# Performance work log

Measured on AMD Instinct MI355X. Metric: run time of the kernel, lower is better.

The kernel has to match this reference:

```python
import jax, jax.numpy as jnp
import numpy as np

# Model dims (from MambaLayer: Mamba2(d_model=256, d_state=128, d_conv=4, expand=2, headdim=64))
D_MODEL = 256
D_INNER = 512
D_STATE = 128
NHEADS = 8
HEADDIM = 64
D_CONV = 4
CONV_DIM = D_INNER + 2 * D_STATE          # 768
D_IN_PROJ = 2 * D_INNER + 2 * D_STATE + NHEADS  # 1288
ATT_HEADS = 8
MLP_HID = 4 * D_MODEL
NUM_CLASSES = 2


def _mamba2(x, in_proj_w, conv_w, conv_b, dt_bias, A_log, D_param, norm_w, out_proj_w):
    """Mamba2 forward (SSD selective scan), ngroups=1, no in_proj/out_proj bias."""
    b, L, _ = x.shape
    zxbcdt = x @ in_proj_w.T                                   # (b,L,1288)
    z = zxbcdt[..., :D_INNER]                                   # gate
    xBC = zxbcdt[..., D_INNER:D_INNER + CONV_DIM]
    dt = jax.nn.softplus(zxbcdt[..., -NHEADS:] + dt_bias)       # (b,L,h)
    # depthwise causal conv1d (kernel 4) + SiLU
    xpad = jnp.pad(xBC, ((0, 0), (D_CONV - 1, 0), (0, 0)))
    xBC = sum(conv_w[:, k] * xpad[:, k:k + L, :] for k in range(D_CONV)) + conv_b
    xBC = jax.nn.silu(xBC)
    xs = xBC[..., :D_INNER].reshape(b, L, NHEADS, HEADDIM)      # (b,L,h,p)
    Bm = xBC[..., D_INNER:D_INNER + D_STATE]                    # (b,L,n)
    Cm = xBC[..., D_INNER + D_STATE:]                           # (b,L,n)
    dA = jnp.exp(dt * (-jnp.exp(A_log)))                        # (b,L,h)

    def step(h_prev, inp):
        dA_t, dt_t, B_t, C_t, x_t = inp                         # (b,h),(b,h),(b,n),(b,n),(b,h,p)
        h = h_prev * dA_t[..., None, None] + (dt_t[..., None] * x_t)[..., None] * B_t[:, None, None, :]
        return h, jnp.einsum('bhpn,bn->bhp', h, C_t)

    tfirst = lambda a: jnp.moveaxis(a, 1, 0)
    h0 = jnp.zeros((b, NHEADS, HEADDIM, D_STATE), x.dtype)
    _, ys = jax.lax.scan(step, h0, (tfirst(dA), tfirst(dt), tfirst(Bm), tfirst(Cm), tfirst(xs)))
    y = jnp.moveaxis(ys, 0, 1) + D_param[None, None, :, None] * xs
    # gated RMSNorm then out projection
    y = y.reshape(b, L, D_INNER) * jax.nn.silu(z)
    y = y * jax.lax.rsqrt(jnp.mean(y * y, -1, keepdims=True) + 1e-5) * norm_w
    return y @ out_proj_w.T


def _cross_attn(x, ctx, wq, wk, wv, wo, wo_b, w1, b1, ln_w, ln_b, w2, b2):
    """CrossModalAttention.forward: attn -> out_proj -> Mlp (no residual, per source)."""
    b, t, c = x.shape
    hd = c // ATT_HEADS
    heads = lambda a: a.reshape(b, -1, ATT_HEADS, hd).transpose(0, 2, 1, 3)
    q, k, v = heads(x @ wq.T), heads(ctx @ wk.T), heads(ctx @ wv.T)
    att = jax.nn.softmax(jnp.einsum('bhxd,bhyd->bhxy', q, k) * (hd ** -0.5), axis=-1)
    o = jnp.einsum('bhxy,bhyd->bhxd', att, v).transpose(0, 2, 1, 3).reshape(b, t, c)
    o = o @ wo.T + wo_b
    h = jax.nn.gelu(o @ w1.T + b1, approximate=False)
    mu = jnp.mean(h, -1, keepdims=True)
    var = jnp.mean((h - mu) ** 2, -1, keepdims=True)
    h = (h - mu) * jax.lax.rsqrt(var + 1e-5) * ln_w + ln_b
    return h @ w2.T + b2


def setup_inputs() -> dict:
    key = jax.random.key(0)
    ks = iter(jax.random.split(key, 32))
    f32 = jnp.float32
    w = lambda *s: jax.random.normal(next(ks), s, f32) * 0.02
    return {
        'x': jax.random.normal(next(ks), (2, 2048, D_MODEL), f32),
        'context': jax.random.normal(next(ks), (2, 2048, D_MODEL), f32),
        'in_proj_w': w(D_IN_PROJ, D_MODEL),
        'conv_w': w(CONV_DIM, D_CONV),
        'conv_b': jnp.zeros((CONV_DIM,), f32),
        'dt_bias': jax.random.normal(next(ks), (NHEADS,), f32) * 0.5,
        'A_log': jnp.log(jnp.linspace(1.0, 16.0, NHEADS).astype(f32)),
        'D_param': jnp.ones((NHEADS,), f32),
        'norm_w': jnp.ones((D_INNER,), f32),
        'out_proj_w': w(D_MODEL, D_INNER),
        'wq': w(D_MODEL, D_MODEL),
        'wk': w(D_MODEL, D_MODEL),
        'wv': w(D_MODEL, D_MODEL),
        'wo': w(D_MODEL, D_MODEL),
        'wo_b': jnp.zeros((D_MODEL,), f32),
        'w1': w(MLP_HID, D_MODEL),
        'b1': jnp.zeros((MLP_HID,), f32),
        'ln_w': jnp.ones((MLP_HID,), f32),
        'ln_b': jnp.zeros((MLP_HID,), f32),
        'w2': w(D_MODEL, MLP_HID),
        'b2': jnp.zeros((D_MODEL,), f32),
        'head_w': w(NUM_CLASSES, D_MODEL),
        'head_b': jnp.zeros((NUM_CLASSES,), f32),
    }


def reference(x, context, in_proj_w, conv_w, conv_b, dt_bias, A_log, D_param, norm_w, out_proj_w,
              wq, wk, wv, wo, wo_b, w1, b1, ln_w, ln_b, w2, b2, head_w, head_b):
    h = x + _mamba2(x, in_proj_w, conv_w, conv_b, dt_bias, A_log, D_param, norm_w, out_proj_w)
    h = _cross_attn(h, context, wq, wk, wv, wo, wo_b, w1, b1, ln_w, ln_b, w2, b2)
    # ClsHead: mean-pool over tokens, linear to classes
    return jnp.mean(h, axis=1) @ head_w.T + head_b
```

## Files before the change

kernel.cpp:

```cpp
#include <hip/hip_runtime.h>
#include <hip/hip_bf16.h>
#include <math.h>

#define DEVFN __device__ __forceinline__

constexpr int BATCH = 2;
constexpr int SEQ   = 2048;
constexpr int DM    = 256;
constexpr int DI    = 512;
constexpr int DSTATE= 128;
constexpr int NH    = 8;
constexpr int HD    = 64;
constexpr int CDIM  = 768;
constexpr int DPROJ = 1288;
constexpr int MTOK  = BATCH*SEQ;
constexpr int HID   = 1024;
constexpr int CHUNK = 32;
constexpr int NCHUNK= SEQ/CHUNK;
constexpr int NSPLIT= 4;
constexpr int KVLEN = SEQ/NSPLIT;

typedef __bf16 bf16x8 __attribute__((ext_vector_type(8)));
typedef __bf16 bf16x4 __attribute__((ext_vector_type(4)));
typedef __bf16 bf16x2 __attribute__((ext_vector_type(2)));
typedef float  f32x4  __attribute__((ext_vector_type(4)));

DEVFN float gelu_exact(float x){ return 0.5f*x*(1.f+erff(x*0.70710678118654752f)); }
DEVFN float silu_f(float x){ return x/(1.f+expf(-x)); }

DEVFN bf16x8 pack8(float4 a, float4 b){
  bf16x8 r;
  r[0]=(__bf16)a.x; r[1]=(__bf16)a.y; r[2]=(__bf16)a.z; r[3]=(__bf16)a.w;
  r[4]=(__bf16)b.x; r[5]=(__bf16)b.y; r[6]=(__bf16)b.z; r[7]=(__bf16)b.w;
  return r;
}
DEVFN f32x4 mfma16(bf16x8 a, bf16x8 b, f32x4 c){
  return __builtin_amdgcn_mfma_f32_16x16x32_bf16(a, b, c, 0, 0, 0);
}

template<int ACT, bool HASBIAS, bool AF32>
__global__ __launch_bounds__(256)
void gemm128(const void* __restrict__ Av, const float* __restrict__ W,
             const float* __restrict__ bias, __bf16* __restrict__ C,
             int M, int N, int K)
{
  __shared__ __bf16 As[128][40];
  __shared__ __bf16 Ws[128][40];
  const int tid = threadIdx.x;
  const int bm = blockIdx.x * 128, bn = blockIdx.y * 128;
  const int wv = tid >> 6, lane = tid & 63;
  const int quad = lane >> 4, mr = lane & 15;
  const int wm = (wv >> 1) * 64, wn = (wv & 1) * 64;
  const int srow = tid >> 2;
  const int skc  = (tid & 3) * 8;

  const float*  af0 = (const float*)Av + (size_t)(bm + srow)*K + skc;
  const float*  af1 = (const float*)Av + (size_t)(bm + srow + 64)*K + skc;
  const __bf16* ab0 = (const __bf16*)Av + (size_t)(bm + srow)*K + skc;
  const __bf16* ab1 = (const __bf16*)Av + (size_t)(bm + srow + 64)*K + skc;
  const bool wok0 = (bn + srow) < N;
  const bool wok1 = (bn + srow + 64) < N;
  const float* wp0 = W + (size_t)(bn + srow)*K + skc;
  const float* wp1 = W + (size_t)(bn + srow + 64)*K + skc;

  bf16x8 A0, A1;
  if (AF32){
    A0 = pack8(*(const float4*)af0, *(const float4*)(af0+4));
    A1 = pack8(*(const float4*)af1, *(const float4*)(af1+4));
  } else {
    A0 = *(const bf16x8*)ab0;
    A1 = *(const bf16x8*)ab1;
  }
  float4 z4 = make_float4(0,0,0,0);
  float4 W00 = wok0 ? *(const float4*)wp0     : z4;
  float4 W01 = wok0 ? *(const float4*)(wp0+4) : z4;
  float4 W10 = wok1 ? *(const float4*)wp1     : z4;
  float4 W11 = wok1 ? *(const float4*)(wp1+4) : z4;

  f32x4 acc[4][4];
  #pragma unroll
  for (int i=0;i<4;i++)
    #pragma unroll
    for (int j=0;j<4;j++) acc[i][j] = f32x4{0.f,0.f,0.f,0.f};

  for (int k0 = 0; k0 < K; k0 += 32) {
    __syncthreads();
    *(bf16x8*)&As[srow   ][skc] = A0;
    *(bf16x8*)&As[srow+64][skc] = A1;
    *(bf16x8*)&Ws[srow   ][skc] = pack8(W00, W01);
    *(bf16x8*)&Ws[srow+64][skc] = pack8(W10, W11);
    __syncthreads();
    if (k0 + 32 < K){
      int kn = k0 + 32;
      if (AF32){
        A0 = pack8(*(const float4*)(af0+kn), *(const float4*)(af0+kn+4));
        A1 = pack8(*(const float4*)(af1+kn), *(const float4*)(af1+kn+4));
      } else {
        A0 = *(const bf16x8*)(ab0+kn);
        A1 = *(const bf16x8*)(ab1+kn);
      }
      W00 = wok0 ? *(const float4*)(wp0+kn)   : z4;
      W01 = wok0 ? *(const float4*)(wp0+kn+4) : z4;
      W10 = wok1 ? *(const float4*)(wp1+kn)   : z4;
      W11 = wok1 ? *(const float4*)(wp1+kn+4) : z4;
    }
    bf16x8 afr[4], bfr[4];
    #pragma unroll
    for (int i=0;i<4;i++) afr[i] = *(const bf16x8*)&As[wm + i*16 + mr][quad*8];
    #pragma unroll
    for (int j=0;j<4;j++) bfr[j] = *(const bf16x8*)&Ws[wn + j*16 + mr][quad*8];
    #pragma unroll
    for (int i=0;i<4;i++)
      #pragma unroll
      for (int j=0;j<4;j++)
        acc[i][j] = mfma16(afr[i], bfr[j], acc[i][j]);
  }

  #pragma unroll
  for (int j=0;j<4;j++){
    int col = bn + wn + j*16 + mr;
    if (col >= N) continue;
    float bb = HASBIAS ? bias[col] : 0.f;
    #pragma unroll
    for (int i=0;i<4;i++){
      #pragma unroll
      for (int reg=0; reg<4; reg++){
        int row = bm + wm + i*16 + quad*4 + reg;
        float vv = acc[i][j][reg] + bb;
        if (ACT == 1) vv = gelu_exact(vv);
        C[(size_t)row*N + col] = (__bf16)vv;
      }
    }
  }
}

__global__ __launch_bounds__(256)
void gemm_outproj(const __bf16* __restrict__ A, const float* __restrict__ W,
                  const float* __restrict__ residf, __bf16* __restrict__ Cb,
                  int M, int N, int K)
{
  __shared__ __bf16 As[64][40];
  __shared__ __bf16 Ws[64][40];
  const int tid = threadIdx.x;
  const int bm = blockIdx.x*64, bn = blockIdx.y*64;
  const int w = tid >> 6, lane = tid & 63;
  const int quad = lane >> 4, mr = lane & 15;
  const int wm = (w >> 1) * 32, wn = (w & 1) * 32;
  const int srow = tid >> 2, skc = (tid & 3) * 8;

  const __bf16* ap = A + (size_t)(bm + srow)*K + skc;
  const float*  wp = W + (size_t)(bn + srow)*K + skc;
  bf16x8 a0 = *(const bf16x8*)ap;
  float4 w0 = *(const float4*)wp, w1 = *(const float4*)(wp+4);

  f32x4 acc[2][2];
  #pragma unroll
  for (int i=0;i<2;i++)
    #pragma unroll
    for (int j=0;j<2;j++) acc[i][j] = f32x4{0.f,0.f,0.f,0.f};

  for (int k0 = 0; k0 < K; k0 += 32){
    __syncthreads();
    *(bf16x8*)&As[srow][skc] = a0;
    *(bf16x8*)&Ws[srow][skc] = pack8(w0, w1);
    __syncthreads();
    if (k0 + 32 < K){
      a0 = *(const bf16x8*)(ap+k0+32);
      w0 = *(const float4*)(wp+k0+32); w1 = *(const float4*)(wp+k0+36);
    }
    bf16x8 af[2], bfr[2];
    af[0]  = *(const bf16x8*)&As[wm      + mr][quad*8];
    af[1]  = *(const bf16x8*)&As[wm + 16 + mr][quad*8];
    bfr[0] = *(const bf16x8*)&Ws[wn      + mr][quad*8];
    bfr[1] = *(const bf16x8*)&Ws[wn + 16 + mr][quad*8];
    #pragma unroll
    for (int i=0;i<2;i++)
      #pragma unroll
      for (int j=0;j<2;j++)
        acc[i][j] = mfma16(af[i], bfr[j], acc[i][j]);
  }

  #pragma unroll
  for (int j=0;j<2;j++){
    int col = bn + wn + j*16 + mr;
    #pragma unroll
    for (int i=0;i<2;i++)
      #pragma unroll
      for (int reg=0;reg<4;reg++){
        int row = bm + wm + i*16 + quad*4 + reg;
        float vv = acc[i][j][reg] + residf[(size_t)row*N + col];
        Cb[(size_t)row*N + col] = (__bf16)vv;
      }
  }
}

__global__ __launch_bounds__(256)
void qkv_gemm(const __bf16* __restrict__ hres, const float* __restrict__ ctx,
              const float* __restrict__ wq, const float* __restrict__ wk,
              const float* __restrict__ wv, __bf16* __restrict__ qo,
              __bf16* __restrict__ ko, __bf16* __restrict__ vt)
{
  __shared__ __bf16 As[64][40];
  __shared__ __bf16 Ws[64][40];
  const int tid = threadIdx.x;
  const int bm = blockIdx.x*64, bn = blockIdx.y*64, z = blockIdx.z;
  const int K = DM, N = DM;
  const bool abf = (z == 0);
  const float*  W = (z == 0) ? wq : (z == 1) ? wk : wv;
  const int w = tid >> 6, lane = tid & 63;
  const int quad = lane >> 4, mr = lane & 15;
  const int wm = (w >> 1) * 32, wn = (w & 1) * 32;
  const int srow = tid >> 2, skc = (tid & 3) * 8;

  const __bf16* apb = hres + (size_t)(bm + srow)*K + skc;
  const float*  apf = ctx  + (size_t)(bm + srow)*K + skc;
  const float*  wp  = W + (size_t)(bn + srow)*K + skc;
  bf16x8 a0;
  if (abf) a0 = *(const bf16x8*)apb;
  else     a0 = pack8(*(const float4*)apf, *(const float4*)(apf+4));
  float4 w0 = *(const float4*)wp, w1 = *(const float4*)(wp+4);

  f32x4 acc[2][2];
  #pragma unroll
  for (int i=0;i<2;i++)
    #pragma unroll
    for (int j=0;j<2;j++) acc[i][j] = f32x4{0.f,0.f,0.f,0.f};

  for (int k0 = 0; k0 < K; k0 += 32){
    __syncthreads();
    *(bf16x8*)&As[srow][skc] = a0;
    *(bf16x8*)&Ws[srow][skc] = pack8(w0, w1);
    __syncthreads();
    if (k0 + 32 < K){
      if (abf) a0 = *(const bf16x8*)(apb+k0+32);
      else     a0 = pack8(*(const float4*)(apf+k0+32), *(const float4*)(apf+k0+36));
      w0 = *(const float4*)(wp+k0+32); w1 = *(const float4*)(wp+k0+36);
    }
    bf16x8 af[2], bfr[2];
    af[0]  = *(const bf16x8*)&As[wm      + mr][quad*8];
    af[1]  = *(const bf16x8*)&As[wm + 16 + mr][quad*8];
    bfr[0] = *(const bf16x8*)&Ws[wn      + mr][quad*8];
    bfr[1] = *(const bf16x8*)&Ws[wn + 16 + mr][quad*8];
    #pragma unroll
    for (int i=0;i<2;i++)
      #pragma unroll
      for (int j=0;j<2;j++)
        acc[i][j] = mfma16(af[i], bfr[j], acc[i][j]);
  }

  if (z < 2){
    __bf16* C = (z == 0) ? qo : ko;
    #pragma unroll
    for (int j=0;j<2;j++){
      int col = bn + wn + j*16 + mr;
      #pragma unroll
      for (int i=0;i<2;i++)
        #pragma unroll
        for (int reg=0;reg<4;reg++){
          int row = bm + wm + i*16 + quad*4 + reg;
          C[(size_t)row*N + col] = (__bf16)acc[i][j][reg];
        }
    }
  } else {
    #pragma unroll
    for (int j=0;j<2;j++){
      int col = bn + wn + j*16 + mr;
      int h = col >> 5, dl = col & 31;
      #pragma unroll
      for (int i=0;i<2;i++){
        int rowb = bm + wm + i*16 + quad*4;
        int b = rowb >> 11, t = rowb & 2047;
        bf16x4 o;
        #pragma unroll
        for (int reg=0;reg<4;reg++) o[reg] = (__bf16)acc[i][j][reg];
        *(bf16x4*)(vt + ((size_t)(b*NH + h)*32 + dl)*SEQ + t) = o;
      }
    }
  }
}

__global__ __launch_bounds__(256)
void wo_gemm(const float* __restrict__ opart, const float* __restrict__ lpart,
             const float* __restrict__ W, const float* __restrict__ bias,
             __bf16* __restrict__ Cb)
{
  __shared__ __bf16 As[64][40];
  __shared__ __bf16 Ws[64][40];
  const int tid = threadIdx.x;
  const int bm = blockIdx.x*64, bn = blockIdx.y*64;
  const int K = DM, N = DM;
  const int w = tid >> 6, lane = tid & 63;
  const int quad = lane >> 4, mr = lane & 15;
  const int wm = (w >> 1) * 32, wn = (w & 1) * 32;
  const int srow = tid >> 2, skc = (tid & 3) * 8;

  const int row = bm + srow;
  const int b = row >> 11, t = row & 2047;
  const float* wp = W + (size_t)(bn + srow)*K + skc;

  f32x4 acc[2][2];
  #pragma unroll
  for (int i=0;i<2;i++)
    #pragma unroll
    for (int j=0;j<2;j++) acc[i][j] = f32x4{0.f,0.f,0.f,0.f};

  for (int k0 = 0; k0 < K; k0 += 32){
    __syncthreads();
    {
      int col = k0 + skc;
      int h = col >> 5;
      float lsum = 0.f;
      #pragma unroll
      for (int s=0;s<NSPLIT;s++)
        lsum += lpart[((size_t)s*16 + b*8 + h)*SEQ + t];
      float inv = 1.f / lsum;
      float va[8] = {0,0,0,0,0,0,0,0};
      #pragma unroll
      for (int s=0;s<NSPLIT;s++){
        const float* op = opart + ((size_t)s*MTOK + row)*DM + col;
        float4 u0 = *(const float4*)op;
        float4 u1 = *(const float4*)(op+4);
        va[0]+=u0.x; va[1]+=u0.y; va[2]+=u0.z; va[3]+=u0.w;
        va[4]+=u1.x; va[5]+=u1.y; va[6]+=u1.z; va[7]+=u1.w;
      }
      bf16x8 a;
      #pragma unroll
      for (int e=0;e<8;e++) a[e] = (__bf16)(va[e]*inv);
      *(bf16x8*)&As[srow][skc] = a;
      float4 w0 = *(const float4*)(wp+k0);
      float4 w1 = *(const float4*)(wp+k0+4);
      *(bf16x8*)&Ws[srow][skc] = pack8(w0, w1);
    }
    __syncthreads();
    bf16x8 af[2], bfr[2];
    af[0]  = *(const bf16x8*)&As[wm      + mr][quad*8];
    af[1]  = *(const bf16x8*)&As[wm + 16 + mr][quad*8];
    bfr[0] = *(const bf16x8*)&Ws[wn      + mr][quad*8];
    bfr[1] = *(const bf16x8*)&Ws[wn + 16 + mr][quad*8];
    #pragma unroll
    for (int i=0;i<2;i++)
      #pragma unroll
      for (int j=0;j<2;j++)
        acc[i][j] = mfma16(af[i], bfr[j], acc[i][j]);
  }

  #pragma unroll
  for (int j=0;j<2;j++){
    int col = bn + wn + j*16 + mr;
    float bb = bias[col];
    #pragma unroll
    for (int i=0;i<2;i++)
      #pragma unroll
      for (int reg=0;reg<4;reg++){
        int r2 = bm + wm + i*16 + quad*4 + reg;
        Cb[(size_t)r2*N + col] = (__bf16)(acc[i][j][reg] + bb);
      }
  }
}

__global__ __launch_bounds__(256)
void conv_dt_kernel(const __bf16* __restrict__ zx, const float* __restrict__ convw,
                    const float* __restrict__ convb, const float* __restrict__ dt_bias,
                    const float* __restrict__ A_log, __bf16* __restrict__ xBC,
                    float* __restrict__ dtb, float* __restrict__ ldab)
{
  int idx = blockIdx.x*256 + threadIdx.x;
  int c = idx % CDIM;
  int bt = idx / CDIM;
  int b = bt >> 11, t = bt & 2047;
  float4 w4 = *(const float4*)(convw + c*4);
  const float* wp = (const float*)&w4;
  float acc = convb[c];
  #pragma unroll
  for (int k=0;k<4;k++){
    int ts = t - 3 + k;
    if (ts >= 0)
      acc = fmaf(wp[k], (float)zx[(size_t)(b*SEQ + ts)*DPROJ + DI + c], acc);
  }
  xBC[(size_t)bt*CDIM + c] = (__bf16)silu_f(acc);
  if (c < NH){
    float raw = (float)zx[(size_t)bt*DPROJ + 2*DI + 2*DSTATE + c] + dt_bias[c];
    float dt = fmaxf(raw, 0.f) + log1pf(expf(-fabsf(raw)));
    int o = (b*NH + c)*SEQ + t;
    dtb[o]  = dt;
    ldab[o] = -__expf(A_log[c]) * dt;
  }
}

__global__ __launch_bounds__(256)
void chunk_state(const __bf16* __restrict__ xBC, const float* __restrict__ dtb,
                 const float* __restrict__ ldab, __bf16* __restrict__ Hc,
                 float* __restrict__ Ac)
{
  const int blk = blockIdx.x;
  const int ch = blk & 63, bh = blk >> 6;
  const int b = bh >> 3, h = bh & 7;
  const int t0 = ch*CHUNK;
  const int tid = threadIdx.x;
  __shared__ float csS[CHUNK], wendS[CHUNK];
  __shared__ __bf16 Xw[64][40];
  __shared__ __bf16 Bt[128][40];

  if (tid < 32){
    float v  = ldab[bh*SEQ + t0 + tid];
    float dtv = dtb[bh*SEQ + t0 + tid];
    #pragma unroll
    for (int off=1; off<32; off<<=1){
      float o = __shfl_up(v, off, 32);
      if (tid >= off) v += o;
    }
    csS[tid] = v;
    float cs31 = __shfl(v, 31, 32);
    wendS[tid] = __expf(cs31 - v) * dtv;
  }
  __syncthreads();
  {
    int s  = tid >> 3;
    int pg = (tid & 7) * 8;
    bf16x8 xv = *(const bf16x8*)(xBC + (size_t)(b*SEQ + t0 + s)*CDIM + h*HD + pg);
    float wgt = wendS[s];
    #pragma unroll
    for (int e=0;e<8;e++) Xw[pg+e][s] = (__bf16)((float)xv[e] * wgt);
    int ng = (tid & 7) * 16;
    const __bf16* bp = xBC + (size_t)(b*SEQ + t0 + s)*CDIM + DI + ng;
    bf16x8 b0 = *(const bf16x8*)bp;
    bf16x8 b1 = *(const bf16x8*)(bp+8);
    #pragma unroll
    for (int e=0;e<8;e++){ Bt[ng+e][s] = b0[e]; Bt[ng+8+e][s] = b1[e]; }
  }
  if (tid == 0) Ac[blk] = __expf(csS[31]);
  __syncthreads();

  const int w = tid >> 6, lane = tid & 63, quad = lane >> 4, mr = lane & 15;
  bf16x8 af = *(const bf16x8*)&Xw[w*16 + mr][quad*8];
  __bf16* out = Hc + (size_t)blk*8192;
  #pragma unroll
  for (int j=0;j<8;j++){
    bf16x8 bfm = *(const bf16x8*)&Bt[j*16 + mr][quad*8];
    f32x4 a = mfma16(af, bfm, f32x4{0.f,0.f,0.f,0.f});
    #pragma unroll
    for (int reg=0; reg<4; reg++){
      int p = w*16 + quad*4 + reg;
      out[p*128 + j*16 + mr] = (__bf16)a[reg];
    }
  }
}

__global__ __launch_bounds__(256)
void state_prefix(__bf16* __restrict__ Hc, const float* __restrict__ Ac)
{
  const int blk = blockIdx.x;
  const int bh = blk >> 4, sub = blk & 15;
  const int tid = threadIdx.x;
  const int off = sub*512 + tid*2;
  __shared__ float AcS[64];
  if (tid < 64) AcS[tid] = Ac[bh*64 + tid];
  __bf16* base = Hc + (size_t)bh*64*8192 + off;
  bf16x2 v[64];
  #pragma unroll
  for (int c=0;c<64;c++) v[c] = *(const bf16x2*)(base + (size_t)c*8192);
  __syncthreads();
  float r0 = 0.f, r1 = 0.f;
  #pragma unroll
  for (int c=0;c<64;c++){
    bf16x2 o; o[0] = (__bf16)r0; o[1] = (__bf16)r1;
    *(bf16x2*)(base + (size_t)c*8192) = o;
    float a = AcS[c];
    r0 = fmaf(a, r0, (float)v[c][0]);
    r1 = fmaf(a, r1, (float)v[c][1]);
  }
}

__global__ __launch_bounds__(256)
void chunk_out(const __bf16* __restrict__ xBC, const float* __restrict__ dtb,
               const float* __restrict__ ldab, const __bf16* __restrict__ h0buf,
               const float* __restrict__ Dparam, __bf16* __restrict__ ybuf)
{
  const int blk = blockIdx.x;
  const int ch = blk & 63, bh = blk >> 6;
  const int b = bh >> 3, h = bh & 7;
  const int t0 = ch*CHUNK;
  const int tid = threadIdx.x;
  __shared__ float csS[CHUNK], dtS[CHUNK];
  __shared__ __bf16 Xct[64][40];
  __shared__ __bf16 Ms[32][40];

  if (tid < 32){
    float v = ldab[bh*SEQ + t0 + tid];
    dtS[tid] = dtb[bh*SEQ + t0 + tid];
    #pragma unroll
    for (int off=1; off<32; off<<=1){
      float o = __shfl_up(v, off, 32);
      if (tid >= off) v += o;
    }
    csS[tid] = v;
  }
  __syncthreads();
  {
    int s  = tid >> 3;
    int pg = (tid & 7) * 8;
    bf16x8 xv = *(const bf16x8*)(xBC + (size_t)(b*SEQ + t0 + s)*CDIM + h*HD + pg);
    #pragma unroll
    for (int e=0;e<8;e++) Xct[pg+e][s] = xv[e];
  }

  const int w = tid >> 6, lane = tid & 63, quad = lane >> 4, mr = lane & 15;
  const int ti = w >> 1, si = w & 1;

  const __bf16* Crow = xBC + (size_t)(b*SEQ + t0 + ti*16 + mr)*CDIM + DI + DSTATE;
  bf16x8 af[4];
  #pragma unroll
  for (int kk=0; kk<4; kk++)
    af[kk] = *(const bf16x8*)(Crow + kk*32 + quad*8);
  f32x4 sacc = f32x4{0.f,0.f,0.f,0.f};
  const __bf16* Brow = xBC + (size_t)(b*SEQ + t0 + si*16 + mr)*CDIM + DI;
  #pragma unroll
  for (int kk=0; kk<4; kk++){
    bf16x8 bfm = *(const bf16x8*)(Brow + kk*32 + quad*8);
    sacc = mfma16(af[kk], bfm, sacc);
  }
  #pragma unroll
  for (int reg=0; reg<4; reg++){
    int t = ti*16 + quad*4 + reg;
    int s = si*16 + mr;
    float m = 0.f;
    if (s <= t) m = __expf(csS[t] - csS[s]) * dtS[s] * sacc[reg];
    Ms[t][s] = (__bf16)m;
  }
  __syncthreads();

  f32x4 acc[2] = { f32x4{0.f,0.f,0.f,0.f}, f32x4{0.f,0.f,0.f,0.f} };
  const __bf16* h0r = h0buf + (size_t)blk*8192;
  #pragma unroll
  for (int j=0;j<2;j++){
    int p = (si*2 + j)*16 + mr;
    #pragma unroll
    for (int kk=0; kk<4; kk++){
      bf16x8 bh0 = *(const bf16x8*)(h0r + (size_t)p*128 + kk*32 + quad*8);
      acc[j] = mfma16(af[kk], bh0, acc[j]);
    }
  }
  #pragma unroll
  for (int reg=0;reg<4;reg++){
    int t = ti*16 + quad*4 + reg;
    float e = __expf(csS[t]);
    acc[0][reg] *= e;
    acc[1][reg] *= e;
  }
  bf16x8 am = *(const bf16x8*)&Ms[ti*16 + mr][quad*8];
  #pragma unroll
  for (int j=0;j<2;j++){
    int p = (si*2 + j)*16 + mr;
    bf16x8 bx = *(const bf16x8*)&Xct[p][quad*8];
    acc[j] = mfma16(am, bx, acc[j]);
  }
  const float Dv = Dparam[h];
  #pragma unroll
  for (int j=0;j<2;j++){
    int p = (si*2 + j)*16 + mr;
    #pragma unroll
    for (int reg=0;reg<4;reg++){
      int t = t0 + ti*16 + quad*4 + reg;
      float xv = (float)xBC[(size_t)(b*SEQ + t)*CDIM + h*HD + p];
      ybuf[(size_t)(b*SEQ + t)*DI + h*HD + p] = (__bf16)fmaf(Dv, xv, acc[j][reg]);
    }
  }
}

__global__ __launch_bounds__(128)
void rmsgate_kernel(__bf16* __restrict__ y, const __bf16* __restrict__ zx,
                    const float* __restrict__ normw)
{
  const int row = blockIdx.x, tid = threadIdx.x;
  const __bf16* zrow = zx + (size_t)row*DPROJ;
  __bf16* yrow = y + (size_t)row*DI;
  bf16x4 yv = *(const bf16x4*)(yrow + tid*4);
  bf16x4 zv = *(const bf16x4*)(zrow + tid*4);
  float g[4];
  float ss = 0.f;
  #pragma unroll
  for (int e=0;e<4;e++){
    g[e] = (float)yv[e] * silu_f((float)zv[e]);
    ss += g[e]*g[e];
  }
  #pragma unroll
  for (int off=1; off<64; off<<=1) ss += __shfl_xor(ss, off);
  __shared__ float red[2];
  if ((tid & 63)==0) red[tid>>6] = ss;
  __syncthreads();
  float tot = red[0] + red[1];
  float rs = rsqrtf(tot * (1.f/DI) + 1e-5f);
  float4 nw = *(const float4*)(normw + tid*4);
  const float* nwp = (const float*)&nw;
  bf16x4 o;
  #pragma unroll
  for (int e=0;e<4;e++) o[e] = (__bf16)(g[e]*rs*nwp[e]);
  *(bf16x4*)(yrow + tid*4) = o;
}

__global__ __launch_bounds__(256)
void flash_part(const __bf16* __restrict__ qb, const __bf16* __restrict__ kb,
                const __bf16* __restrict__ vt, float* __restrict__ opart,
                float* __restrict__ lpart)
{
  const int qt = blockIdx.x, ksp = blockIdx.y, bh = blockIdx.z;
  const int b = bh >> 3, h = bh & 7;
  const int tid = threadIdx.x;
  const int w = tid >> 6, lane = tid & 63;
  const int quad = lane >> 4, mr = lane & 15;
  const int qrow0 = b*SEQ + qt*128 + w*32;
  const float SC = 0.17677669529663687f;
  __shared__ __bf16 Pq[4][32][72];

  bf16x8 bq[2];
  #pragma unroll
  for (int i2=0;i2<2;i2++)
    bq[i2] = *(const bf16x8*)(qb + (size_t)(qrow0 + i2*16 + mr)*DM + h*32 + quad*8);

  f32x4 accO[2][2];
  #pragma unroll
  for (int i=0;i<2;i++)
    #pragma unroll
    for (int j=0;j<2;j++) accO[i][j] = f32x4{0.f,0.f,0.f,0.f};
  float lacc[2] = {0.f, 0.f};

  for (int kt=0; kt<KVLEN/64; kt++){
    const int kbase = b*SEQ + ksp*KVLEN + kt*64;
    float tl[2] = {0.f, 0.f};
    #pragma unroll
    for (int ik=0; ik<4; ik++){
      bf16x8 ak = *(const bf16x8*)(kb + (size_t)(kbase + ik*16 + mr)*DM + h*32 + quad*8);
      #pragma unroll
      for (int jq=0; jq<2; jq++){
        f32x4 st = mfma16(ak, bq[jq], f32x4{0.f,0.f,0.f,0.f});
        bf16x4 e4;
        float sa = 0.f;
        #pragma unroll
        for (int reg=0; reg<4; reg++){
          float e = __expf(st[reg] * SC);
          sa += e;
          e4[reg] = (__bf16)e;
        }
        tl[jq] += sa;
        *(bf16x4*)&Pq[w][jq*16 + mr][ik*16 + quad*4] = e4;
      }
    }
    #pragma unroll
    for (int jq=0; jq<2; jq++){
      float v = tl[jq];
      v += __shfl_xor(v, 16);
      v += __shfl_xor(v, 32);
      lacc[jq] += v;
    }
    #pragma unroll
    for (int ks=0; ks<2; ks++){
      bf16x8 pa0 = *(const bf16x8*)&Pq[w][     mr][ks*32 + quad*8];
      bf16x8 pa1 = *(const bf16x8*)&Pq[w][16 + mr][ks*32 + quad*8];
      #pragma unroll
      for (int j2=0; j2<2; j2++){
        bf16x8 bv = *(const bf16x8*)(vt + ((size_t)bh*32 + j2*16 + mr)*SEQ
                        + ksp*KVLEN + kt*64 + ks*32 + quad*8);
        accO[0][j2] = mfma16(pa0, bv, accO[0][j2]);
        accO[1][j2] = mfma16(pa1, bv, accO[1][j2]);
      }
    }
  }

  #pragma unroll
  for (int i2=0;i2<2;i2++)
    #pragma unroll
    for (int j2=0;j2<2;j2++)
      #pragma unroll
      for (int reg=0;reg<4;reg++){
        int row = qrow0 + i2*16 + quad*4 + reg;
        opart[((size_t)ksp*MTOK + row)*DM + h*32 + j2*16 + mr] = accO[i2][j2][reg];
      }
  if (quad == 0){
    #pragma unroll
    for (int jq=0;jq<2;jq++)
      lpart[((size_t)ksp*16 + bh)*SEQ + (qt*128 + w*32 + jq*16 + mr)] = lacc[jq];
  }
}

__global__ __launch_bounds__(256)
void lnorm_kernel(__bf16* __restrict__ hb, const float* __restrict__ lnw,
                  const float* __restrict__ lnb)
{
  const int row = blockIdx.x, tid = threadIdx.x;
  __bf16* hr = hb + (size_t)row*HID;
  bf16x4 v4 = *(const bf16x4*)(hr + tid*4);
  float v[4];
  float sum = 0.f, sq = 0.f;
  #pragma unroll
  for (int e=0;e<4;e++){ v[e] = (float)v4[e]; sum += v[e]; sq += v[e]*v[e]; }
  #pragma unroll
  for (int off=1; off<64; off<<=1){ sum += __shfl_xor(sum,off); sq += __shfl_xor(sq,off); }
  __shared__ float s1[4], s2[4];
  int w = tid>>6;
  if ((tid & 63)==0){ s1[w]=sum; s2[w]=sq; }
  __syncthreads();
  sum = (s1[0]+s1[1])+(s1[2]+s1[3]);
  sq  = (s2[0]+s2[1])+(s2[2]+s2[3]);
  float mu = sum * (1.f/HID);
  float var = sq * (1.f/HID) - mu*mu;
  float rstd = rsqrtf(var + 1e-5f);
  float4 wv = *(const float4*)(lnw + tid*4);
  float4 bv = *(const float4*)(lnb + tid*4);
  const float* wp = (const float*)&wv;
  const float* bp = (const float*)&bv;
  bf16x4 o;
  #pragma unroll
  for (int e=0;e<4;e++) o[e] = (__bf16)((v[e]-mu)*rstd*wp[e] + bp[e]);
  *(bf16x4*)(hr + tid*4) = o;
}

__global__ __launch_bounds__(256)
void pool_ln(const __bf16* __restrict__ h1, float* __restrict__ pp)
{
  const int blk = blockIdx.x;
  const int b = blk >> 6, seg = blk & 63;
  const int tid = threadIdx.x;
  const int c4 = tid*4;
  float4 s = make_float4(0,0,0,0);
  const __bf16* basep = h1 + ((size_t)(b*SEQ + seg*32))*HID + c4;
  #pragma unroll 4
  for (int r=0;r<32;r++){
    bf16x4 v = *(const bf16x4*)(basep + (size_t)r*HID);
    s.x += (float)v[0]; s.y += (float)v[1]; s.z += (float)v[2]; s.w += (float)v[3];
  }
  *(float4*)(pp + ((size_t)(b*64+seg))*HID + c4) = s;
}

__global__ __launch_bounds__(256)
void head2_kernel(const float* __restrict__ pp, const float* __restrict__ w2,
                  const float* __restrict__ b2, const float* __restrict__ hw,
                  const float* __restrict__ hb, float* __restrict__ out)
{
  const int b = blockIdx.x, tid = threadIdx.x;
  __shared__ float pooled[HID];
  __shared__ float w2h[DM];
  {
    int c4 = tid*4;
    float4 s = make_float4(0,0,0,0);
    #pragma unroll 4
    for (int seg=0;seg<64;seg++){
      float4 v = *(const float4*)(pp + ((size_t)(b*64+seg))*HID + c4);
      s.x+=v.x; s.y+=v.y; s.z+=v.z; s.w+=v.w;
    }
    const float inv = 1.f/(float)SEQ;
    *(float4*)&pooled[c4] = make_float4(s.x*inv, s.y*inv, s.z*inv, s.w*inv);
  }
  __syncthreads();
  {
    float acc = 0.f;
    const float* wr = w2 + (size_t)tid*HID;
    #pragma unroll 8
    for (int k=0;k<HID;k+=4){
      float4 wv4 = *(const float4*)(wr+k);
      float4 pv  = *(const float4*)&pooled[k];
      acc += wv4.x*pv.x + wv4.y*pv.y + wv4.z*pv.z + wv4.w*pv.w;
    }
    w2h[tid] = acc + b2[tid];
  }
  __syncthreads();
  if (tid < 128){
    int cls = tid >> 6, lane = tid & 63;
    float acc = 0.f;
    for (int c=lane;c<DM;c+=64) acc += w2h[c]*hw[cls*DM+c];
    #pragma unroll
    for (int off=1;off<64;off<<=1) acc += __shfl_xor(acc, off);
    if (lane == 0) out[b*2 + cls] = acc + hb[cls];
  }
}

extern "C" void kernel_launch(void* const* d_in, const int* in_sizes, int n_in,
                              void* d_out, int out_size, void* d_ws, size_t ws_size,
                              hipStream_t stream)
{
  const float* x         = (const float*)d_in[0];
  const float* context   = (const float*)d_in[1];
  const float* in_proj_w = (const float*)d_in[2];
  const float* conv_w    = (const float*)d_in[3];
  const float* conv_b    = (const float*)d_in[4];
  const float* dt_bias   = (const float*)d_in[5];
  const float* A_log     = (const float*)d_in[6];
  const float* D_param   = (const float*)d_in[7];
  const float* norm_w    = (const float*)d_in[8];
  const float* out_proj_w= (const float*)d_in[9];
  const float* wq  = (const float*)d_in[10];
  const float* wk  = (const float*)d_in[11];
  const float* wv  = (const float*)d_in[12];
  const float* wo  = (const float*)d_in[13];
  const float* wo_b= (const float*)d_in[14];
  const float* w1  = (const float*)d_in[15];
  const float* b1  = (const float*)d_in[16];
  const float* ln_w= (const float*)d_in[17];
  const float* ln_b= (const float*)d_in[18];
  const float* w2  = (const float*)d_in[19];
  const float* b2  = (const float*)d_in[20];
  const float* head_w = (const float*)d_in[21];
  const float* head_b = (const float*)d_in[22];
  float* out = (float*)d_out;
  float* ws  = (float*)d_ws;

  __bf16* zx    = (__bf16*)ws;
  __bf16* xBC   = (__bf16*)(ws + 2637824);
  float* dtb    = ws + 4210688;
  float* ldab   = ws + 4243456;
  __bf16* Hcb   = (__bf16*)(ws + 4276224);
  float* Acb    = ws + 8470528;
  __bf16* ybuf  = (__bf16*)(ws + 8471552);
  __bf16* hres  = (__bf16*)(ws + 9520128);
  __bf16* qbf   = (__bf16*)(ws + 10044416);
  __bf16* kbf   = (__bf16*)(ws + 10568704);
  __bf16* vtbf  = (__bf16*)(ws + 11092992);
  float* opart  = ws + 11617280;
  float* lpart  = ws + 15811584;
  __bf16* o2bf  = (__bf16*)(ws + 15942656);
  __bf16* h1bf  = (__bf16*)(ws + 4276224);
  float* poolp  = ws + 11617280;

  const dim3 g64(MTOK/64, DM/64);

  gemm128<0,false,true><<<dim3(MTOK/128, (DPROJ+127)/128), dim3(256), 0, stream>>>(
      x, in_proj_w, nullptr, zx, MTOK, DPROJ, DM);
  conv_dt_kernel<<<dim3(MTOK*CDIM/256), dim3(256), 0, stream>>>(
      zx, conv_w, conv_b, dt_bias, A_log, xBC, dtb, ldab);
  chunk_state<<<dim3(BATCH*NH*NCHUNK), dim3(256), 0, stream>>>(
      xBC, dtb, ldab, Hcb, Acb);
  state_prefix<<<dim3(256), dim3(256), 0, stream>>>(Hcb, Acb);
  chunk_out<<<dim3(BATCH*NH*NCHUNK), dim3(256), 0, stream>>>(
      xBC, dtb, ldab, Hcb, D_param, ybuf);
  rmsgate_kernel<<<dim3(MTOK), dim3(128), 0, stream>>>(ybuf, zx, norm_w);
  gemm_outproj<<<g64, dim3(256), 0, stream>>>(
      ybuf, out_proj_w, x, hres, MTOK, DM, DI);
  qkv_gemm<<<dim3(MTOK/64, DM/64, 3), dim3(256), 0, stream>>>(
      hres, context, wq, wk, wv, qbf, kbf, vtbf);
  flash_part<<<dim3(SEQ/128, NSPLIT, BATCH*NH), dim3(256), 0, stream>>>(
      qbf, kbf, vtbf, opart, lpart);
  wo_gemm<<<g64, dim3(256), 0, stream>>>(opart, lpart, wo, wo_b, o2bf);
  gemm128<1,true,false><<<dim3(MTOK/128, HID/128), dim3(256), 0, stream>>>(
      o2bf, w1, b1, h1bf, MTOK, HID, DM);
  lnorm_kernel<<<dim3(MTOK), dim3(256), 0, stream>>>(h1bf, ln_w, ln_b);
  pool_ln<<<dim3(128), dim3(256), 0, stream>>>(h1bf, poolp);
  head2_kernel<<<dim3(BATCH), dim3(256), 0, stream>>>(
      poolp, w2, b2, head_w, head_b, out);
  (void)in_sizes; (void)n_in; (void)out_size; (void)ws_size;
}
```

Before: 320.6 us.

## Pre-convert weights to bf16, fuse layernorm with pooling, split flash combine

Adds a kernel that converts all projection weights to bf16 once per call, so the GEMMs load bf16 weights directly instead of packing fp32 on every tile. It also halves the flash-attention KV split count, moves the split combine out of the wo GEMM into its own kernel, fuses the layernorm into the pooling pass so the normalized activations are never written back, and vectorizes the conv/dt kernel to four channels per thread. The cost is an extra conversion launch and an extra combine launch, plus fewer attention blocks for parallelism.

```diff
diff --git a/kernel.cpp b/kernel.cpp
--- a/kernel.cpp
+++ b/kernel.cpp
@@ -17,8 +17,17 @@
 constexpr int HID   = 1024;
 constexpr int CHUNK = 32;
 constexpr int NCHUNK= SEQ/CHUNK;
-constexpr int NSPLIT= 4;
+constexpr int NSPLIT= 2;
 constexpr int KVLEN = SEQ/NSPLIT;
+
+constexpr int W_INPROJ = 0;
+constexpr int W_OUTPROJ= 329728;
+constexpr int W_Q      = 460800;
+constexpr int W_K      = 526336;
+constexpr int W_V      = 591872;
+constexpr int W_O      = 657408;
+constexpr int W_1      = 722944;
+constexpr int W_TOT    = 985088;
 
 typedef __bf16 bf16x8 __attribute__((ext_vector_type(8)));
 typedef __bf16 bf16x4 __attribute__((ext_vector_type(4)));
@@ -38,9 +47,30 @@
   return __builtin_amdgcn_mfma_f32_16x16x32_bf16(a, b, c, 0, 0, 0);
 }
 
+__global__ __launch_bounds__(256)
+void cvt_w(const float* __restrict__ w_inproj, const float* __restrict__ w_outproj,
+           const float* __restrict__ wq, const float* __restrict__ wk,
+           const float* __restrict__ wv, const float* __restrict__ wo,
+           const float* __restrict__ w1, __bf16* __restrict__ wbf)
+{
+  int i4 = (blockIdx.x*256 + threadIdx.x)*4;
+  const float* src;
+  if      (i4 < W_OUTPROJ) src = w_inproj  + i4;
+  else if (i4 < W_Q)       src = w_outproj + (i4 - W_OUTPROJ);
+  else if (i4 < W_K)       src = wq + (i4 - W_Q);
+  else if (i4 < W_V)       src = wk + (i4 - W_K);
+  else if (i4 < W_O)       src = wv + (i4 - W_V);
+  else if (i4 < W_1)       src = wo + (i4 - W_O);
+  else                     src = w1 + (i4 - W_1);
+  float4 v = *(const float4*)src;
+  bf16x4 o;
+  o[0]=(__bf16)v.x; o[1]=(__bf16)v.y; o[2]=(__bf16)v.z; o[3]=(__bf16)v.w;
+  *(bf16x4*)(wbf + i4) = o;
+}
+
 template<int ACT, bool HASBIAS, bool AF32>
 __global__ __launch_bounds__(256)
-void gemm128(const void* __restrict__ Av, const float* __restrict__ W,
+void gemm128(const void* __restrict__ Av, const __bf16* __restrict__ W,
              const float* __restrict__ bias, __bf16* __restrict__ C,
              int M, int N, int K)
 {
@@ -60,9 +90,10 @@
   const __bf16* ab1 = (const __bf16*)Av + (size_t)(bm + srow + 64)*K + skc;
   const bool wok0 = (bn + srow) < N;
   const bool wok1 = (bn + srow + 64) < N;
-  const float* wp0 = W + (size_t)(bn + srow)*K + skc;
-  const float* wp1 = W + (size_t)(bn + srow + 64)*K + skc;
-
+  const __bf16* wp0 = W + (size_t)(bn + srow)*K + skc;
+  const __bf16* wp1 = W + (size_t)(bn + srow + 64)*K + skc;
+
+  bf16x8 zb{};
   bf16x8 A0, A1;
   if (AF32){
     A0 = pack8(*(const float4*)af0, *(const float4*)(af0+4));
@@ -71,11 +102,8 @@
     A0 = *(const bf16x8*)ab0;
     A1 = *(const bf16x8*)ab1;
   }
-  float4 z4 = make_float4(0,0,0,0);
-  float4 W00 = wok0 ? *(const float4*)wp0     : z4;
-  float4 W01 = wok0 ? *(const float4*)(wp0+4) : z4;
-  float4 W10 = wok1 ? *(const float4*)wp1     : z4;
-  float4 W11 = wok1 ? *(const float4*)(wp1+4) : z4;
+  bf16x8 W0 = wok0 ? *(const bf16x8*)wp0 : zb;
+  bf16x8 W1 = wok1 ? *(const bf16x8*)wp1 : zb;
 
   f32x4 acc[4][4];
   #pragma unroll
@@ -87,8 +115,8 @@
     __syncthreads();
     *(bf16x8*)&As[srow   ][skc] = A0;
     *(bf16x8*)&As[srow+64][skc] = A1;
-    *(bf16x8*)&Ws[srow   ][skc] = pack8(W00, W01);
-    *(bf16x8*)&Ws[srow+64][skc] = pack8(W10, W11);
+    *(bf16x8*)&Ws[srow   ][skc] = W0;
+    *(bf16x8*)&Ws[srow+64][skc] = W1;
     __syncthreads();
     if (k0 + 32 < K){
       int kn = k0 + 32;
@@ -99,10 +127,8 @@
         A0 = *(const bf16x8*)(ab0+kn);
         A1 = *(const bf16x8*)(ab1+kn);
       }
-      W00 = wok0 ? *(const float4*)(wp0+kn)   : z4;
-      W01 = wok0 ? *(const float4*)(wp0+kn+4) : z4;
-      W10 = wok1 ? *(const float4*)(wp1+kn)   : z4;
-      W11 = wok1 ? *(const float4*)(wp1+kn+4) : z4;
+      W0 = wok0 ? *(const bf16x8*)(wp0+kn) : zb;
+      W1 = wok1 ? *(const bf16x8*)(wp1+kn) : zb;
     }
     bf16x8 afr[4], bfr[4];
     #pragma unroll
@@ -134,10 +160,11 @@
   }
 }
 
-__global__ __launch_bounds__(256)
-void gemm_outproj(const __bf16* __restrict__ A, const float* __restrict__ W,
-                  const float* __restrict__ residf, __bf16* __restrict__ Cb,
-                  int M, int N, int K)
+template<bool HASBIAS, bool HASRESF>
+__global__ __launch_bounds__(256)
+void gemm64b(const __bf16* __restrict__ A, const __bf16* __restrict__ W,
+             const float* __restrict__ bias, const float* __restrict__ residf,
+             __bf16* __restrict__ Cb, int M, int N, int K)
 {
   __shared__ __bf16 As[64][40];
   __shared__ __bf16 Ws[64][40];
@@ -149,9 +176,9 @@
   const int srow = tid >> 2, skc = (tid & 3) * 8;
 
   const __bf16* ap = A + (size_t)(bm + srow)*K + skc;
-  const float*  wp = W + (size_t)(bn + srow)*K + skc;
+  const __bf16* wp = W + (size_t)(bn + srow)*K + skc;
   bf16x8 a0 = *(const bf16x8*)ap;
-  float4 w0 = *(const float4*)wp, w1 = *(const float4*)(wp+4);
+  bf16x8 w0 = *(const bf16x8*)wp;
 
   f32x4 acc[2][2];
   #pragma unroll
@@ -162,11 +189,11 @@
   for (int k0 = 0; k0 < K; k0 += 32){
     __syncthreads();
     *(bf16x8*)&As[srow][skc] = a0;
-    *(bf16x8*)&Ws[srow][skc] = pack8(w0, w1);
+    *(bf16x8*)&Ws[srow][skc] = w0;
     __syncthreads();
     if (k0 + 32 < K){
       a0 = *(const bf16x8*)(ap+k0+32);
-      w0 = *(const float4*)(wp+k0+32); w1 = *(const float4*)(wp+k0+36);
+      w0 = *(const bf16x8*)(wp+k0+32);
     }
     bf16x8 af[2], bfr[2];
     af[0]  = *(const bf16x8*)&As[wm      + mr][quad*8];
@@ -183,12 +210,14 @@
   #pragma unroll
   for (int j=0;j<2;j++){
     int col = bn + wn + j*16 + mr;
+    float bb = HASBIAS ? bias[col] : 0.f;
     #pragma unroll
     for (int i=0;i<2;i++)
       #pragma unroll
       for (int reg=0;reg<4;reg++){
         int row = bm + wm + i*16 + quad*4 + reg;
-        float vv = acc[i][j][reg] + residf[(size_t)row*N + col];
+        float vv = acc[i][j][reg] + bb;
+        if (HASRESF) vv += residf[(size_t)row*N + col];
         Cb[(size_t)row*N + col] = (__bf16)vv;
       }
   }
@@ -196,8 +225,7 @@
 
 __global__ __launch_bounds__(256)
 void qkv_gemm(const __bf16* __restrict__ hres, const float* __restrict__ ctx,
-              const float* __restrict__ wq, const float* __restrict__ wk,
-              const float* __restrict__ wv, __bf16* __restrict__ qo,
+              const __bf16* __restrict__ wbf, __bf16* __restrict__ qo,
               __bf16* __restrict__ ko, __bf16* __restrict__ vt)
 {
   __shared__ __bf16 As[64][40];
@@ -206,7 +234,7 @@
   const int bm = blockIdx.x*64, bn = blockIdx.y*64, z = blockIdx.z;
   const int K = DM, N = DM;
   const bool abf = (z == 0);
-  const float*  W = (z == 0) ? wq : (z == 1) ? wk : wv;
+  const __bf16* W = wbf + ((z == 0) ? W_Q : (z == 1) ? W_K : W_V);
   const int w = tid >> 6, lane = tid & 63;
   const int quad = lane >> 4, mr = lane & 15;
   const int wm = (w >> 1) * 32, wn = (w & 1) * 32;
@@ -214,11 +242,11 @@
 
   const __bf16* apb = hres + (size_t)(bm + srow)*K + skc;
   const float*  apf = ctx  + (size_t)(bm + srow)*K + skc;
-  const float*  wp  = W + (size_t)(bn + srow)*K + skc;
+  const __bf16* wp  = W + (size_t)(bn + srow)*K + skc;
   bf16x8 a0;
   if (abf) a0 = *(const bf16x8*)apb;
   else     a0 = pack8(*(const float4*)apf, *(const float4*)(apf+4));
-  float4 w0 = *(const float4*)wp, w1 = *(const float4*)(wp+4);
+  bf16x8 w0 = *(const bf16x8*)wp;
 
   f32x4 acc[2][2];
   #pragma unroll
@@ -229,12 +257,12 @@
   for (int k0 = 0; k0 < K; k0 += 32){
     __syncthreads();
     *(bf16x8*)&As[srow][skc] = a0;
-    *(bf16x8*)&Ws[srow][skc] = pack8(w0, w1);
+    *(bf16x8*)&Ws[srow][skc] = w0;
     __syncthreads();
     if (k0 + 32 < K){
       if (abf) a0 = *(const bf16x8*)(apb+k0+32);
       else     a0 = pack8(*(const float4*)(apf+k0+32), *(const float4*)(apf+k0+36));
-      w0 = *(const float4*)(wp+k0+32); w1 = *(const float4*)(wp+k0+36);
+      w0 = *(const bf16x8*)(wp+k0+32);
     }
     bf16x8 af[2], bfr[2];
     af[0]  = *(const bf16x8*)&As[wm      + mr][quad*8];
@@ -280,110 +308,46 @@
 }
 
 __global__ __launch_bounds__(256)
-void wo_gemm(const float* __restrict__ opart, const float* __restrict__ lpart,
-             const float* __restrict__ W, const float* __restrict__ bias,
-             __bf16* __restrict__ Cb)
-{
-  __shared__ __bf16 As[64][40];
-  __shared__ __bf16 Ws[64][40];
-  const int tid = threadIdx.x;
-  const int bm = blockIdx.x*64, bn = blockIdx.y*64;
-  const int K = DM, N = DM;
-  const int w = tid >> 6, lane = tid & 63;
-  const int quad = lane >> 4, mr = lane & 15;
-  const int wm = (w >> 1) * 32, wn = (w & 1) * 32;
-  const int srow = tid >> 2, skc = (tid & 3) * 8;
-
-  const int row = bm + srow;
-  const int b = row >> 11, t = row & 2047;
-  const float* wp = W + (size_t)(bn + srow)*K + skc;
-
-  f32x4 acc[2][2];
-  #pragma unroll
-  for (int i=0;i<2;i++)
-    #pragma unroll
-    for (int j=0;j<2;j++) acc[i][j] = f32x4{0.f,0.f,0.f,0.f};
-
-  for (int k0 = 0; k0 < K; k0 += 32){
-    __syncthreads();
-    {
-      int col = k0 + skc;
-      int h = col >> 5;
-      float lsum = 0.f;
-      #pragma unroll
-      for (int s=0;s<NSPLIT;s++)
-        lsum += lpart[((size_t)s*16 + b*8 + h)*SEQ + t];
-      float inv = 1.f / lsum;
-      float va[8] = {0,0,0,0,0,0,0,0};
-      #pragma unroll
-      for (int s=0;s<NSPLIT;s++){
-        const float* op = opart + ((size_t)s*MTOK + row)*DM + col;
-        float4 u0 = *(const float4*)op;
-        float4 u1 = *(const float4*)(op+4);
-        va[0]+=u0.x; va[1]+=u0.y; va[2]+=u0.z; va[3]+=u0.w;
-        va[4]+=u1.x; va[5]+=u1.y; va[6]+=u1.z; va[7]+=u1.w;
-      }
-      bf16x8 a;
-      #pragma unroll
-      for (int e=0;e<8;e++) a[e] = (__bf16)(va[e]*inv);
-      *(bf16x8*)&As[srow][skc] = a;
-      float4 w0 = *(const float4*)(wp+k0);
-      float4 w1 = *(const float4*)(wp+k0+4);
-      *(bf16x8*)&Ws[srow][skc] = pack8(w0, w1);
-    }
-    __syncthreads();
-    bf16x8 af[2], bfr[2];
-    af[0]  = *(const bf16x8*)&As[wm      + mr][quad*8];
-    af[1]  = *(const bf16x8*)&As[wm + 16 + mr][quad*8];
-    bfr[0] = *(const bf16x8*)&Ws[wn      + mr][quad*8];
-    bfr[1] = *(const bf16x8*)&Ws[wn + 16 + mr][quad*8];
-    #pragma unroll
-    for (int i=0;i<2;i++)
-      #pragma unroll
-      for (int j=0;j<2;j++)
-        acc[i][j] = mfma16(af[i], bfr[j], acc[i][j]);
-  }
-
-  #pragma unroll
-  for (int j=0;j<2;j++){
-    int col = bn + wn + j*16 + mr;
-    float bb = bias[col];
-    #pragma unroll
-    for (int i=0;i<2;i++)
-      #pragma unroll
-      for (int reg=0;reg<4;reg++){
-        int r2 = bm + wm + i*16 + quad*4 + reg;
-        Cb[(size_t)r2*N + col] = (__bf16)(acc[i][j][reg] + bb);
-      }
-  }
-}
-
-__global__ __launch_bounds__(256)
 void conv_dt_kernel(const __bf16* __restrict__ zx, const float* __restrict__ convw,
                     const float* __restrict__ convb, const float* __restrict__ dt_bias,
                     const float* __restrict__ A_log, __bf16* __restrict__ xBC,
                     float* __restrict__ dtb, float* __restrict__ ldab)
 {
   int idx = blockIdx.x*256 + threadIdx.x;
-  int c = idx % CDIM;
-  int bt = idx / CDIM;
+  int c4 = (idx % (CDIM/4))*4;
+  int bt = idx / (CDIM/4);
   int b = bt >> 11, t = bt & 2047;
-  float4 w4 = *(const float4*)(convw + c*4);
-  const float* wp = (const float*)&w4;
-  float acc = convb[c];
+  float acc[4];
+  float4 cb = *(const float4*)(convb + c4);
+  acc[0]=cb.x; acc[1]=cb.y; acc[2]=cb.z; acc[3]=cb.w;
+  float4 wrow[4];
+  #pragma unroll
+  for (int j=0;j<4;j++) wrow[j] = *(const float4*)(convw + (c4+j)*4);
   #pragma unroll
   for (int k=0;k<4;k++){
     int ts = t - 3 + k;
-    if (ts >= 0)
-      acc = fmaf(wp[k], (float)zx[(size_t)(b*SEQ + ts)*DPROJ + DI + c], acc);
-  }
-  xBC[(size_t)bt*CDIM + c] = (__bf16)silu_f(acc);
-  if (c < NH){
-    float raw = (float)zx[(size_t)bt*DPROJ + 2*DI + 2*DSTATE + c] + dt_bias[c];
-    float dt = fmaxf(raw, 0.f) + log1pf(expf(-fabsf(raw)));
-    int o = (b*NH + c)*SEQ + t;
-    dtb[o]  = dt;
-    ldab[o] = -__expf(A_log[c]) * dt;
+    if (ts >= 0){
+      bf16x4 xv = *(const bf16x4*)(zx + (size_t)(b*SEQ + ts)*DPROJ + DI + c4);
+      const float* wk4[4] = {(const float*)&wrow[0], (const float*)&wrow[1],
+                             (const float*)&wrow[2], (const float*)&wrow[3]};
+      #pragma unroll
+      for (int j=0;j<4;j++) acc[j] = fmaf(wk4[j][k], (float)xv[j], acc[j]);
+    }
+  }
+  bf16x4 o;
+  #pragma unroll
+  for (int j=0;j<4;j++) o[j] = (__bf16)silu_f(acc[j]);
+  *(bf16x4*)(xBC + (size_t)bt*CDIM + c4) = o;
+  if (c4 < NH){
+    #pragma unroll
+    for (int j=0;j<4;j++){
+      int h = c4 + j;
+      float raw = (float)zx[(size_t)bt*DPROJ + 2*DI + 2*DSTATE + h] + dt_bias[h];
+      float dt = fmaxf(raw, 0.f) + log1pf(expf(-fabsf(raw)));
+      int oo = (b*NH + h)*SEQ + t;
+      dtb[oo]  = dt;
+      ldab[oo] = -__expf(A_log[h]) * dt;
+    }
   }
 }
 
@@ -683,52 +647,61 @@
 }
 
 __global__ __launch_bounds__(256)
-void lnorm_kernel(__bf16* __restrict__ hb, const float* __restrict__ lnw,
-                  const float* __restrict__ lnb)
-{
-  const int row = blockIdx.x, tid = threadIdx.x;
-  __bf16* hr = hb + (size_t)row*HID;
-  bf16x4 v4 = *(const bf16x4*)(hr + tid*4);
-  float v[4];
-  float sum = 0.f, sq = 0.f;
-  #pragma unroll
-  for (int e=0;e<4;e++){ v[e] = (float)v4[e]; sum += v[e]; sq += v[e]*v[e]; }
-  #pragma unroll
-  for (int off=1; off<64; off<<=1){ sum += __shfl_xor(sum,off); sq += __shfl_xor(sq,off); }
+void flash_combine(const float* __restrict__ opart, const float* __restrict__ lpart,
+                   __bf16* __restrict__ o)
+{
+  int idx = blockIdx.x*256 + threadIdx.x;
+  int row = idx >> 6, d4 = (idx & 63)*4;
+  int h = d4 >> 5;
+  int b = row >> 11, t = row & 2047;
+  float sx=0.f, sy=0.f, sz=0.f, sw=0.f, lsum=0.f;
+  #pragma unroll
+  for (int s4=0; s4<NSPLIT; s4++){
+    float4 vv = *(const float4*)(opart + ((size_t)s4*MTOK + row)*DM + d4);
+    sx += vv.x; sy += vv.y; sz += vv.z; sw += vv.w;
+    lsum += lpart[((size_t)s4*16 + b*8 + h)*SEQ + t];
+  }
+  float inv = 1.f / lsum;
+  bf16x4 ov;
+  ov[0]=(__bf16)(sx*inv); ov[1]=(__bf16)(sy*inv);
+  ov[2]=(__bf16)(sz*inv); ov[3]=(__bf16)(sw*inv);
+  *(bf16x4*)(o + (size_t)row*DM + d4) = ov;
+}
+
+__global__ __launch_bounds__(256)
+void ln_pool(const __bf16* __restrict__ h1, const float* __restrict__ lnw,
+             const float* __restrict__ lnb, float* __restrict__ pp)
+{
+  const int blk = blockIdx.x;
+  const int tid = threadIdx.x;
+  const int row0 = blk*16;
   __shared__ float s1[4], s2[4];
-  int w = tid>>6;
-  if ((tid & 63)==0){ s1[w]=sum; s2[w]=sq; }
-  __syncthreads();
-  sum = (s1[0]+s1[1])+(s1[2]+s1[3]);
-  sq  = (s2[0]+s2[1])+(s2[2]+s2[3]);
-  float mu = sum * (1.f/HID);
-  float var = sq * (1.f/HID) - mu*mu;
-  float rstd = rsqrtf(var + 1e-5f);
   float4 wv = *(const float4*)(lnw + tid*4);
   float4 bv = *(const float4*)(lnb + tid*4);
   const float* wp = (const float*)&wv;
   const float* bp = (const float*)&bv;
-  bf16x4 o;
-  #pragma unroll
-  for (int e=0;e<4;e++) o[e] = (__bf16)((v[e]-mu)*rstd*wp[e] + bp[e]);
-  *(bf16x4*)(hr + tid*4) = o;
-}
-
-__global__ __launch_bounds__(256)
-void pool_ln(const __bf16* __restrict__ h1, float* __restrict__ pp)
-{
-  const int blk = blockIdx.x;
-  const int b = blk >> 6, seg = blk & 63;
-  const int tid = threadIdx.x;
-  const int c4 = tid*4;
-  float4 s = make_float4(0,0,0,0);
-  const __bf16* basep = h1 + ((size_t)(b*SEQ + seg*32))*HID + c4;
-  #pragma unroll 4
-  for (int r=0;r<32;r++){
-    bf16x4 v = *(const bf16x4*)(basep + (size_t)r*HID);
-    s.x += (float)v[0]; s.y += (float)v[1]; s.z += (float)v[2]; s.w += (float)v[3];
-  }
-  *(float4*)(pp + ((size_t)(b*64+seg))*HID + c4) = s;
+  float acc[4] = {0.f,0.f,0.f,0.f};
+  for (int r=0;r<16;r++){
+    bf16x4 v4 = *(const bf16x4*)(h1 + (size_t)(row0+r)*HID + tid*4);
+    float v[4];
+    float sum=0.f, sq=0.f;
+    #pragma unroll
+    for (int e=0;e<4;e++){ v[e]=(float)v4[e]; sum+=v[e]; sq+=v[e]*v[e]; }
+    #pragma unroll
+    for (int off=1; off<64; off<<=1){ sum += __shfl_xor(sum,off); sq += __shfl_xor(sq,off); }
+    int w = tid>>6;
+    __syncthreads();
+    if ((tid & 63)==0){ s1[w]=sum; s2[w]=sq; }
+    __syncthreads();
+    sum = (s1[0]+s1[1])+(s1[2]+s1[3]);
+    sq  = (s2[0]+s2[1])+(s2[2]+s2[3]);
+    float mu = sum * (1.f/HID);
+    float var = sq * (1.f/HID) - mu*mu;
+    float rstd = rsqrtf(var + 1e-5f);
+    #pragma unroll
+    for (int e=0;e<4;e++) acc[e] += (v[e]-mu)*rstd*wp[e] + bp[e];
+  }
+  *(float4*)(pp + (size_t)blk*HID + tid*4) = make_float4(acc[0],acc[1],acc[2],acc[3]);
 }
 
 __global__ __launch_bounds__(256)
@@ -743,8 +716,8 @@
     int c4 = tid*4;
     float4 s = make_float4(0,0,0,0);
     #pragma unroll 4
-    for (int seg=0;seg<64;seg++){
-      float4 v = *(const float4*)(pp + ((size_t)(b*64+seg))*HID + c4);
+    for (int seg=0;seg<128;seg++){
+      float4 v = *(const float4*)(pp + ((size_t)(b*128+seg))*HID + c4);
       s.x+=v.x; s.y+=v.y; s.z+=v.z; s.w+=v.w;
     }
     const float inv = 1.f/(float)SEQ;
@@ -815,16 +788,20 @@
   __bf16* kbf   = (__bf16*)(ws + 10568704);
   __bf16* vtbf  = (__bf16*)(ws + 11092992);
   float* opart  = ws + 11617280;
-  float* lpart  = ws + 15811584;
-  __bf16* o2bf  = (__bf16*)(ws + 15942656);
+  float* lpart  = ws + 13714432;
+  __bf16* obf   = (__bf16*)(ws + 13779968);
+  __bf16* o2bf  = (__bf16*)(ws + 14304256);
+  __bf16* wbf   = (__bf16*)(ws + 14828544);
   __bf16* h1bf  = (__bf16*)(ws + 4276224);
   float* poolp  = ws + 11617280;
 
   const dim3 g64(MTOK/64, DM/64);
 
+  cvt_w<<<dim3(W_TOT/1024), dim3(256), 0, stream>>>(
+      in_proj_w, out_proj_w, wq, wk, wv, wo, w1, wbf);
   gemm128<0,false,true><<<dim3(MTOK/128, (DPROJ+127)/128), dim3(256), 0, stream>>>(
-      x, in_proj_w, nullptr, zx, MTOK, DPROJ, DM);
-  conv_dt_kernel<<<dim3(MTOK*CDIM/256), dim3(256), 0, stream>>>(
+      x, wbf + W_INPROJ, nullptr, zx, MTOK, DPROJ, DM);
+  conv_dt_kernel<<<dim3(MTOK*CDIM/1024), dim3(256), 0, stream>>>(
       zx, conv_w, conv_b, dt_bias, A_log, xBC, dtb, ldab);
   chunk_state<<<dim3(BATCH*NH*NCHUNK), dim3(256), 0, stream>>>(
       xBC, dtb, ldab, Hcb, Acb);
@@ -832,17 +809,18 @@
   chunk_out<<<dim3(BATCH*NH*NCHUNK), dim3(256), 0, stream>>>(
       xBC, dtb, ldab, Hcb, D_param, ybuf);
   rmsgate_kernel<<<dim3(MTOK), dim3(128), 0, stream>>>(ybuf, zx, norm_w);
-  gemm_outproj<<<g64, dim3(256), 0, stream>>>(
-      ybuf, out_proj_w, x, hres, MTOK, DM, DI);
+  gemm64b<false,true><<<g64, dim3(256), 0, stream>>>(
+      ybuf, wbf + W_OUTPROJ, nullptr, x, hres, MTOK, DM, DI);
   qkv_gemm<<<dim3(MTOK/64, DM/64, 3), dim3(256), 0, stream>>>(
-      hres, context, wq, wk, wv, qbf, kbf, vtbf);
+      hres, context, wbf, qbf, kbf, vtbf);
   flash_part<<<dim3(SEQ/128, NSPLIT, BATCH*NH), dim3(256), 0, stream>>>(
       qbf, kbf, vtbf, opart, lpart);
-  wo_gemm<<<g64, dim3(256), 0, stream>>>(opart, lpart, wo, wo_b, o2bf);
+  flash_combine<<<dim3(MTOK*64/256), dim3(256), 0, stream>>>(opart, lpart, obf);
+  gemm64b<true,false><<<g64, dim3(256), 0, stream>>>(
+      obf, wbf + W_O, wo_b, nullptr, o2bf, MTOK, DM, DM);
   gemm128<1,true,false><<<dim3(MTOK/128, HID/128), dim3(256), 0, stream>>>(
-      o2bf, w1, b1, h1bf, MTOK, HID, DM);
-  lnorm_kernel<<<dim3(MTOK), dim3(256), 0, stream>>>(h1bf, ln_w, ln_b);
-  pool_ln<<<dim3(128), dim3(256), 0, stream>>>(h1bf, poolp);
+      o2bf, wbf + W_1, b1, h1bf, MTOK, HID, DM);
+  ln_pool<<<dim3(256), dim3(256), 0, stream>>>(h1bf, ln_w, ln_b, poolp);
   head2_kernel<<<dim3(BATCH), dim3(256), 0, stream>>>(
       poolp, w2, b2, head_w, head_b, out);
   (void)in_sizes; (void)n_in; (void)out_size; (void)ws_size;
```

Result: faster. 304.3 us (-5.1%).
